# Kernel optimization log

Measured on AMD Instinct MI355X. Metric: run time of the kernel, lower is better.

Reference implementation:

```python
import jax, jax.numpy as jnp
import numpy as np

N = 50000      # nodes
E = 800000     # edges
C = 32         # channels (in = hidden = out, hardcoded in module)
KS = 4         # spline kernel size per dim
K = KS ** 3    # total spline kernel weights (dim=3)
H = 8          # NodeFormer heads
DH = C // H    # head dim = 4
M = 32         # random features for softmax kernel
EPS = 1e-5
SLOPE = 0.01   # LeakyReLU default
TAU = 1.0      # forward default


def seg_sum(vals, segs, num):
    return jax.ops.segment_sum(vals, segs, num_segments=num)


def leaky(x):
    return jnp.where(x >= 0, x, SLOPE * x)


def batch_norm(x, gamma, beta):
    # BatchNorm1d in training mode over the node dim (biased variance)
    mu = x.mean(0)
    var = x.var(0)
    return (x - mu) * jax.lax.rsqrt(var + EPS) * gamma + beta


def spline_conv(x, edge_index, pseudo, w_kernel, w_root, bias):
    # Degree-1 open B-spline conv (torch_spline_conv semantics), mean aggregation.
    src, dst = edge_index[0], edge_index[1]
    x_src = x[src]                                  # [E, C] gather
    p = pseudo * (KS - 1)                           # [E, 3], pseudo in [0,1]
    f = jnp.clip(jnp.floor(p), 0, KS - 2).astype(jnp.int32)
    frac = p - f                                    # [E, 3]
    buf = jnp.zeros((N * K, C), x.dtype)            # [N*K, C] per-kernel scatter buffer
    for bits in range(8):                           # 2^dim nonzero basis products
        idx = jnp.zeros(E, jnp.int32)
        basis = jnp.ones(E, x.dtype)
        for d in range(3):
            bit = (bits >> d) & 1
            idx = idx + (f[:, d] + bit) * (KS ** d)
            basis = basis * (frac[:, d] if bit else (1.0 - frac[:, d]))
        buf = buf + seg_sum(basis[:, None] * x_src, dst.astype(jnp.int32) * K + idx, N * K)
    buf = buf.reshape(N, K, C)
    deg = jnp.clip(seg_sum(jnp.ones(E, x.dtype), dst, N), 1.0)
    out = jnp.einsum('nkc,kcd->nd', buf, w_kernel) / deg[:, None]
    return out + x @ w_root + bias


def softmax_kernel(x, wp):
    # Positive random-feature map approximating the softmax kernel. x: [N,H,DH]
    xn = x / (DH ** 0.25)
    proj = jnp.einsum('nhd,hdm->nhm', xn, wp)
    sq = 0.5 * jnp.sum(xn * xn, -1, keepdims=True)
    return jnp.exp(proj - sq) / np.float32(np.sqrt(M))


def nodeformer_conv(x, edge_index, wqkv, wp, b_rel, wo, bo, gumbel, tau):
    # Kernelized Gumbel-softmax linear attention over all nodes + edge relational bias.
    q = jnp.einsum('nc,chd->nhd', x, wqkv[0])
    k = jnp.einsum('nc,chd->nhd', x, wqkv[1])
    v = jnp.einsum('nc,chd->nhd', x, wqkv[2])
    phi_q = softmax_kernel(q, wp)                              # [N,H,M]
    phi_k = softmax_kernel(k, wp) * jnp.exp(gumbel / tau)      # gumbel: [N,H,1]
    kv = jnp.einsum('nhm,nhd->hmd', phi_k, v)                  # [H,M,DH] summary
    num = jnp.einsum('nhm,hmd->nhd', phi_q, kv)
    den = jnp.einsum('nhm,hm->nh', phi_q, phi_k.sum(0)) + 1e-6
    attn = num / den[..., None]                                # [N,H,DH]
    # relational bias along observed edges (deg-normalized message passing)
    src, dst = edge_index[0], edge_index[1]
    deg = jnp.clip(seg_sum(jnp.ones(E, x.dtype), dst, N), 1.0)
    norm_e = jax.lax.rsqrt(deg[src] * deg[dst])
    rel = seg_sum(v[src] * norm_e[:, None, None], dst, N)      # [N,H,DH]
    out = attn + jax.nn.sigmoid(b_rel)[None, :, None] * rel
    return out.reshape(N, H * DH) @ wo + bo


def setup_inputs() -> dict:
    key = jax.random.key(0)
    ks = jax.random.split(key, 24)
    s_k = np.float32(1.0 / np.sqrt(C))
    inp = {
        'patch_embs': jax.random.normal(ks[0], (N, C), jnp.float32),
        'edge_index': jax.random.randint(ks[1], (2, E), 0, N),
        'edge_attr': jax.random.uniform(ks[2], (E, 3), jnp.float32),
        # SplineConv 1 & 2 params
        'w_sp1': jax.random.normal(ks[3], (K, C, C), jnp.float32) * s_k,
        'root1': jax.random.normal(ks[4], (C, C), jnp.float32) * s_k,
        'bias1': jnp.zeros((C,), jnp.float32),
        'w_sp2': jax.random.normal(ks[5], (K, C, C), jnp.float32) * s_k,
        'root2': jax.random.normal(ks[6], (C, C), jnp.float32) * s_k,
        'bias2': jnp.zeros((C,), jnp.float32),
        # 4 BatchNorm layers, packed
        'bn_gamma': jnp.ones((4, C), jnp.float32),
        'bn_beta': jnp.zeros((4, C), jnp.float32),
        # NodeFormer layer 1
        'nf1_wqkv': jax.random.normal(ks[7], (3, C, H, DH), jnp.float32) * s_k,
        'nf1_wp': jax.random.normal(ks[8], (H, DH, M), jnp.float32),
        'nf1_brel': jnp.zeros((H,), jnp.float32),
        'nf1_wo': jax.random.normal(ks[9], (H * DH, C), jnp.float32) * s_k,
        'nf1_bo': jnp.zeros((C,), jnp.float32),
        'gumbel1': -jnp.log(-jnp.log(jax.random.uniform(ks[10], (N, H, 1), jnp.float32) + 1e-9) + 1e-9),
        # NodeFormer layer 2
        'nf2_wqkv': jax.random.normal(ks[11], (3, C, H, DH), jnp.float32) * s_k,
        'nf2_wp': jax.random.normal(ks[12], (H, DH, M), jnp.float32),
        'nf2_brel': jnp.zeros((H,), jnp.float32),
        'nf2_wo': jax.random.normal(ks[13], (H * DH, C), jnp.float32) * s_k,
        'nf2_bo': jnp.zeros((C,), jnp.float32),
        'gumbel2': -jnp.log(-jnp.log(jax.random.uniform(ks[14], (N, H, 1), jnp.float32) + 1e-9) + 1e-9),
    }
    return inp


def reference(patch_embs, edge_index, edge_attr,
              w_sp1, root1, bias1, w_sp2, root2, bias2,
              bn_gamma, bn_beta,
              nf1_wqkv, nf1_wp, nf1_brel, nf1_wo, nf1_bo, gumbel1,
              nf2_wqkv, nf2_wp, nf2_brel, nf2_wo, nf2_bo, gumbel2):
    x = batch_norm(leaky(spline_conv(patch_embs, edge_index, edge_attr, w_sp1, root1, bias1)), bn_gamma[0], bn_beta[0])
    x = batch_norm(leaky(spline_conv(x, edge_index, edge_attr, w_sp2, root2, bias2)), bn_gamma[1], bn_beta[1])
    x = batch_norm(leaky(nodeformer_conv(x, edge_index, nf1_wqkv, nf1_wp, nf1_brel, nf1_wo, nf1_bo, gumbel1, TAU)), bn_gamma[2], bn_beta[2])
    x = batch_norm(nodeformer_conv(x, edge_index, nf2_wqkv, nf2_wp, nf2_brel, nf2_wo, nf2_bo, gumbel2, TAU), bn_gamma[3], bn_beta[3])
    return x
```

## Files before the change

### kernel.cpp

```cpp
#include <hip/hip_runtime.h>
#include <hip/hip_bf16.h>

#define NN 50000
#define NE 800000

__device__ __forceinline__ void gAdd(float* p, float v) {
    unsafeAtomicAdd(p, v);
}
__device__ __forceinline__ unsigned short f2bf(float f) {
    unsigned u = __float_as_uint(f);
    u += 0x7FFF + ((u >> 16) & 1);
    return (unsigned short)(u >> 16);
}

__global__ void k_hist(const int* __restrict__ ei, int* __restrict__ cnt) {
    int e = blockIdx.x * 256 + threadIdx.x;
    atomicAdd(&cnt[ei[NE + e]], 1);
}

__global__ void __launch_bounds__(1024) k_scan(const int* __restrict__ cnt,
                                               int* __restrict__ rowptr,
                                               int* __restrict__ fill,
                                               float* __restrict__ degf) {
    __shared__ int wsum[16];
    int tid = threadIdx.x;
    int wave = tid >> 6, lane = tid & 63;
    int carry = 0;
    for (int base = 0; base < NN; base += 8192) {
        int i0 = base + tid * 8;
        int v[8], pre[8], s = 0;
#pragma unroll
        for (int j = 0; j < 8; j++) {
            int i = i0 + j;
            v[j] = (i < NN) ? cnt[i] : 0;
            pre[j] = s; s += v[j];
        }
        int sc = s;
#pragma unroll
        for (int d = 1; d < 64; d <<= 1) {
            int t = __shfl_up(sc, d);
            if (lane >= d) sc += t;
        }
        if (lane == 63) wsum[wave] = sc;
        __syncthreads();
        int wpre = 0, total = 0;
#pragma unroll
        for (int w = 0; w < 16; w++) {
            int x = wsum[w];
            if (w < wave) wpre += x;
            total += x;
        }
        int excl = carry + wpre + (sc - s);
#pragma unroll
        for (int j = 0; j < 8; j++) {
            int i = i0 + j;
            if (i < NN) {
                int st = excl + pre[j];
                rowptr[i] = st;
                fill[i]   = st;
                degf[i]   = (float)(v[j] > 0 ? v[j] : 1);
                if (i == NN - 1) rowptr[NN] = st + v[j];
            }
        }
        carry += total;
        __syncthreads();
    }
}

__global__ void k_scatter(const int* __restrict__ ei, const float* __restrict__ attr,
                          const float* __restrict__ degf,
                          int* __restrict__ fill, float4* __restrict__ sedge,
                          float2* __restrict__ re2) {
    int e = blockIdx.x * 256 + threadIdx.x;
    int src = ei[e], dst = ei[NE + e];
    int pos = atomicAdd(&fill[dst], 1);
    float4 r;
    r.x = __int_as_float(src);
    r.y = attr[e * 3 + 0]; r.z = attr[e * 3 + 1]; r.w = attr[e * 3 + 2];
    sedge[pos] = r;
    re2[pos] = make_float2(__int_as_float(src), rsqrtf(degf[src] * degf[dst]));
}

__global__ void k_cvt(const float* __restrict__ xin, unsigned short* __restrict__ xh) {
    int i = blockIdx.x * 256 + threadIdx.x;
    xh[i] = f2bf(xin[i]);
}

__device__ __forceinline__ void edge_rmw(float* __restrict__ buf,
                                         float ay, float az, float aw, int t,
                                         float xs, int ch, int hi) {
    float p0 = ay * 3.f, p1 = az * 3.f, p2 = aw * 3.f;
    float f0 = fmaxf(fminf(floorf(p0), 2.f), 0.f);
    float f1 = fmaxf(fminf(floorf(p1), 2.f), 0.f);
    float f2 = fmaxf(fminf(floorf(p2), 2.f), 0.f);
    float r0 = p0 - f0, r1 = p1 - f1, r2 = p2 - f2;
    int i0 = (int)f0, i1 = (int)f1, i2 = (int)f2;
    int addr0, addr1, addr2, addr3;
    float b0v, b1v, b2v, b3v;
#pragma unroll
    for (int q = 0; q < 4; q++) {
        int bits = hi * 4 + q;
        int b0 = bits & 1, b1 = (bits >> 1) & 1, b2 = (bits >> 2) & 1;
        float bas = (b0 ? r0 : 1.f - r0) * (b1 ? r1 : 1.f - r1) * (b2 ? r2 : 1.f - r2);
        int idx = (i0 + b0) + 4 * (i1 + b1) + 16 * (i2 + b2);
        int a = ((idx * 4 + t) << 5) + (ch ^ ((idx & 7) << 2));
        if (q == 0) { addr0 = a; b0v = bas * xs; }
        else if (q == 1) { addr1 = a; b1v = bas * xs; }
        else if (q == 2) { addr2 = a; b2v = bas * xs; }
        else { addr3 = a; b3v = bas * xs; }
    }
    float v0 = buf[addr0], v1 = buf[addr1], v2 = buf[addr2], v3 = buf[addr3];
    buf[addr0] = v0 + b0v;
    buf[addr1] = v1 + b1v;
    buf[addr2] = v2 + b2v;
    buf[addr3] = v3 + b3v;
}

__global__ void __launch_bounds__(256) k_spline(
        const float* __restrict__ xin, const unsigned short* __restrict__ xh,
        const int* __restrict__ rowptr,
        const float4* __restrict__ sedge, const float* __restrict__ degf,
        const float* __restrict__ wsp, const float* __restrict__ root,
        const float* __restrict__ bias, float* __restrict__ out,
        float* __restrict__ stats) {
    __shared__ __align__(16) float buf[8192];
    __shared__ __align__(16) float xt[4][32];
    __shared__ __align__(16) float scr[1024];
    __shared__ float scr2[2][64];
    int tid = threadIdx.x;
    int wave = tid >> 6, lane = tid & 63;
    for (int i = tid; i < 8192; i += 256) buf[i] = 0.f;
    int nb = blockIdx.x * 4;
    if (tid < 128) {
        int t = tid >> 5, c = tid & 31;
        xt[t][c] = xin[(nb + t) * 32 + c];
    }
    __syncthreads();
    {
        int n = nb + wave;
        int rs = rowptr[n], re = rowptr[n + 1];
        int ch = lane & 31, hi = lane >> 5;
        for (int ce = rs; ce < re; ce += 64) {
            int cnt = re - ce; if (cnt > 64) cnt = 64;
            float4 myed = make_float4(0.f, 0.f, 0.f, 0.f);
            if (lane < cnt) myed = sedge[ce + lane];
            int mysrc = __float_as_int(myed.x);
            for (int j0 = 0; j0 < cnt; j0 += 8) {
                float xsv[8], ey[8], ez[8], ew[8];
#pragma unroll
                for (int jj = 0; jj < 8; jj++) {
                    int j = j0 + jj;
                    int s  = __shfl(mysrc, j);
                    ey[jj] = __shfl(myed.y, j);
                    ez[jj] = __shfl(myed.z, j);
                    ew[jj] = __shfl(myed.w, j);
                    int sc = (j < cnt) ? s : 0;
                    unsigned short u = xh[sc * 32 + ch];
                    xsv[jj] = __uint_as_float(((unsigned)u) << 16);
                }
#pragma unroll
                for (int jj = 0; jj < 8; jj++) {
                    int j = j0 + jj;
                    if (j < cnt)
                        edge_rmw(buf, ey[jj], ez[jj], ew[jj], wave, xsv[jj], ch, hi);
                }
            }
        }
    }
    __syncthreads();
    int kk = lane >> 3, d8 = lane & 7;
    float4 acc[2][4];
#pragma unroll
    for (int hf = 0; hf < 2; hf++)
#pragma unroll
        for (int t = 0; t < 4; t++) acc[hf][t] = make_float4(0.f, 0.f, 0.f, 0.f);
#pragma unroll
    for (int hf = 0; hf < 2; hf++) {
        int k = hf * 32 + wave * 8 + kk;
        const float* wk = wsp + k * 1024;
#pragma unroll
        for (int c4 = 0; c4 < 8; c4++) {
            float4 wv0 = *(const float4*)(wk + (c4 * 4 + 0) * 32 + d8 * 4);
            float4 wv1 = *(const float4*)(wk + (c4 * 4 + 1) * 32 + d8 * 4);
            float4 wv2 = *(const float4*)(wk + (c4 * 4 + 2) * 32 + d8 * 4);
            float4 wv3 = *(const float4*)(wk + (c4 * 4 + 3) * 32 + d8 * 4);
            int cp = (c4 ^ kk) << 2;
            const float* bp = &buf[(k * 4) << 5];
#pragma unroll
            for (int t = 0; t < 4; t++) {
                float4 bv = *(const float4*)(bp + (t << 5) + cp);
                acc[hf][t].x += bv.x * wv0.x + bv.y * wv1.x + bv.z * wv2.x + bv.w * wv3.x;
                acc[hf][t].y += bv.x * wv0.y + bv.y * wv1.y + bv.z * wv2.y + bv.w * wv3.y;
                acc[hf][t].z += bv.x * wv0.z + bv.y * wv1.z + bv.z * wv2.z + bv.w * wv3.z;
                acc[hf][t].w += bv.x * wv0.w + bv.y * wv1.w + bv.z * wv2.w + bv.w * wv3.w;
            }
        }
    }
#pragma unroll
    for (int hf = 0; hf < 2; hf++)
#pragma unroll
    for (int t = 0; t < 4; t++) {
        float sx = acc[hf][t].x, sy = acc[hf][t].y, sz = acc[hf][t].z, sw = acc[hf][t].w;
        sx += __shfl_xor(sx, 8);  sy += __shfl_xor(sy, 8);  sz += __shfl_xor(sz, 8);  sw += __shfl_xor(sw, 8);
        sx += __shfl_xor(sx, 16); sy += __shfl_xor(sy, 16); sz += __shfl_xor(sz, 16); sw += __shfl_xor(sw, 16);
        sx += __shfl_xor(sx, 32); sy += __shfl_xor(sy, 32); sz += __shfl_xor(sz, 32); sw += __shfl_xor(sw, 32);
        acc[hf][t] = make_float4(sx, sy, sz, sw);
    }
    if (kk == 0) {
#pragma unroll
        for (int hf = 0; hf < 2; hf++)
#pragma unroll
        for (int t = 0; t < 4; t++)
            *(float4*)&scr[(wave * 2 + hf) * 128 + d8 * 16 + t * 4] = acc[hf][t];
    }
    __syncthreads();
    if (tid < 128) {
        int t = tid >> 5, d = tid & 31;
        int n = nb + t;
        float v = 0.f;
#pragma unroll
        for (int wh = 0; wh < 8; wh++)
            v += scr[wh * 128 + (d >> 2) * 16 + t * 4 + (d & 3)];
        v /= degf[n];
        float rt = 0.f;
#pragma unroll
        for (int c = 0; c < 32; c++) rt += xt[t][c] * root[c * 32 + d];
        v += rt + bias[d];
        v = v >= 0.f ? v : 0.01f * v;
        out[n * 32 + d] = v;
        float s = v, s2 = v * v;
        s += __shfl_xor(s, 32); s2 += __shfl_xor(s2, 32);
        if ((tid & 63) < 32) {
            scr2[tid >> 6][d] = s;
            scr2[tid >> 6][32 + d] = s2;
        }
    }
    __syncthreads();
    if (tid < 64) gAdd(&stats[(blockIdx.x & 63) * 64 + tid], scr2[0][tid] + scr2[1][tid]);
}

__global__ void k_red(const float* __restrict__ stats, float* __restrict__ fin) {
    int j = threadIdx.x;
    float s = 0.f;
#pragma unroll 8
    for (int r = 0; r < 64; r++) s += stats[r * 64 + j];
    fin[j] = s;
}

__global__ void k_bn(const float* __restrict__ tin, const float* __restrict__ fin,
                     const float* __restrict__ gamma, const float* __restrict__ beta,
                     float* __restrict__ xout) {
    int i = blockIdx.x * 256 + threadIdx.x;
    int c = i & 31;
    float mu = fin[c] * (1.f / NN);
    float var = fin[32 + c] * (1.f / NN) - mu * mu;
    float g = gamma[c] * rsqrtf(var + 1e-5f);
    xout[i] = (tin[i] - mu) * g + beta[c];
}
__global__ void k_bn_cvt(const float* __restrict__ tin, const float* __restrict__ fin,
                         const float* __restrict__ gamma, const float* __restrict__ beta,
                         float* __restrict__ xout, unsigned short* __restrict__ xh) {
    int i = blockIdx.x * 256 + threadIdx.x;
    int c = i & 31;
    float mu = fin[c] * (1.f / NN);
    float var = fin[32 + c] * (1.f / NN) - mu * mu;
    float g = gamma[c] * rsqrtf(var + 1e-5f);
    float v = (tin[i] - mu) * g + beta[c];
    xout[i] = v;
    xh[i] = f2bf(v);
}

__global__ void __launch_bounds__(256) k_nf1(
        const float* __restrict__ x, const float* __restrict__ wqkv,
        const float* __restrict__ wp, const float* __restrict__ gumbel,
        float* __restrict__ vbuf, float* __restrict__ kvg) {
    __shared__ float xl[32 * 33];
    __shared__ __align__(16) float kq[32][8][4];
    __shared__ __align__(16) float vv[32][8][4];
    __shared__ float sqv[32][8];
    __shared__ float gsv[32][8];
    int tid = threadIdx.x;
    int base = blockIdx.x * 32;
#pragma unroll
    for (int r = 0; r < 4; r++) {
        int i = r * 256 + tid;
        int gi = base * 32 + i;
        float v = (gi < NN * 32) ? x[gi] : 0.f;
        xl[(i >> 5) * 33 + (i & 31)] = v;
    }
    __syncthreads();
    int nl = tid >> 3, h = tid & 7;
    int n = base + nl;
    int act = (n < NN) ? 1 : 0;
    const float* xp = &xl[nl * 33];
    float kr0 = 0, kr1 = 0, kr2 = 0, kr3 = 0, vr0 = 0, vr1 = 0, vr2 = 0, vr3 = 0;
#pragma unroll
    for (int c = 0; c < 32; c++) {
        float xc = xp[c];
        const float4 wk4 = *(const float4*)(wqkv + 1024 + c * 32 + h * 4);
        const float4 wv4 = *(const float4*)(wqkv + 2048 + c * 32 + h * 4);
        kr0 += xc * wk4.x; kr1 += xc * wk4.y; kr2 += xc * wk4.z; kr3 += xc * wk4.w;
        vr0 += xc * wv4.x; vr1 += xc * wv4.y; vr2 += xc * wv4.z; vr3 += xc * wv4.w;
    }
    if (act) *(float4*)&vbuf[n * 32 + h * 4] = make_float4(vr0, vr1, vr2, vr3);
    const float inv_rt2 = 0.70710678118f;
    const float invSqM = 0.17677669529f;
    float x0 = kr0 * inv_rt2, x1 = kr1 * inv_rt2, x2 = kr2 * inv_rt2, x3 = kr3 * inv_rt2;
    float sq = 0.5f * (x0 * x0 + x1 * x1 + x2 * x2 + x3 * x3);
    float gs = act ? (__expf(gumbel[(act ? n : 0) * 8 + h]) * invSqM) : 0.f;
    *(float4*)&kq[nl][h][0] = make_float4(x0, x1, x2, x3);
    *(float4*)&vv[nl][h][0] = make_float4(vr0, vr1, vr2, vr3);
    sqv[nl][h] = sq;
    gsv[nl][h] = gs;
    __syncthreads();
    int h2 = tid >> 5, m = tid & 31;
    const float* wph = wp + h2 * 128;
    float w0 = wph[m], w1 = wph[32 + m], w2 = wph[64 + m], w3 = wph[96 + m];
    float ks = 0.f, a0 = 0.f, a1 = 0.f, a2 = 0.f, a3 = 0.f;
#pragma unroll 4
    for (int nn2 = 0; nn2 < 32; nn2++) {
        float4 k4 = *(const float4*)&kq[nn2][h2][0];
        float4 v4 = *(const float4*)&vv[nn2][h2][0];
        float pr = k4.x * w0 + k4.y * w1 + k4.z * w2 + k4.w * w3;
        float phk = __expf(pr - sqv[nn2][h2]) * gsv[nn2][h2];
        ks += phk;
        a0 += phk * v4.x; a1 += phk * v4.y; a2 += phk * v4.z; a3 += phk * v4.w;
    }
    float* kvr = kvg + (blockIdx.x & 7) * 1280;
    gAdd(&kvr[1024 + h2 * 32 + m], ks);
    gAdd(&kvr[0 * 256 + h2 * 32 + m], a0);
    gAdd(&kvr[1 * 256 + h2 * 32 + m], a1);
    gAdd(&kvr[2 * 256 + h2 * 32 + m], a2);
    gAdd(&kvr[3 * 256 + h2 * 32 + m], a3);
}

__global__ void __launch_bounds__(256) k_nf2(
        const float* __restrict__ x, const float* __restrict__ wqkv,
        const float* __restrict__ wp, const float* __restrict__ brel,
        const float* __restrict__ wo, const float* __restrict__ bo,
        const float* __restrict__ kvg, const int* __restrict__ rowptr,
        const float2* __restrict__ re2, const float* __restrict__ vbuf,
        int do_leaky, float* __restrict__ out, float* __restrict__ stats) {
    __shared__ float xl[32 * 33];
    __shared__ float ylds[32 * 33];
    __shared__ float kvs[1280];
    __shared__ float scr2[4][64];
    int tid = threadIdx.x;
    int base = blockIdx.x * 32;
#pragma unroll
    for (int r = 0; r < 4; r++) {
        int i = r * 256 + tid;
        int gi = base * 32 + i;
        float v = (gi < NN * 32) ? x[gi] : 0.f;
        xl[(i >> 5) * 33 + (i & 31)] = v;
    }
    for (int i = tid; i < 1280; i += 256) {
        float s = 0.f;
#pragma unroll
        for (int r = 0; r < 8; r++) s += kvg[r * 1280 + i];
        kvs[i] = s;
    }
    __syncthreads();
    int nl = tid >> 3, h = tid & 7;
    int n = base + nl;
    int act = (n < NN) ? 1 : 0;
    int nc = act ? n : (NN - 1);
    const float* xp = &xl[nl * 33];
    float q0 = 0, q1 = 0, q2 = 0, q3 = 0;
#pragma unroll
    for (int c = 0; c < 32; c++) {
        float xc = xp[c];
        const float4 wq4 = *(const float4*)(wqkv + c * 32 + h * 4);
        q0 += xc * wq4.x; q1 += xc * wq4.y; q2 += xc * wq4.z; q3 += xc * wq4.w;
    }
    const float inv_rt2 = 0.70710678118f;
    const float invSqM = 0.17677669529f;
    float x0 = q0 * inv_rt2, x1 = q1 * inv_rt2, x2 = q2 * inv_rt2, x3 = q3 * inv_rt2;
    float sq = 0.5f * (x0 * x0 + x1 * x1 + x2 * x2 + x3 * x3);
    const float* wph = wp + h * 128;
    float den = 0.f, n0 = 0.f, n1 = 0.f, n2 = 0.f, n3 = 0.f;
    for (int mm = 0; mm < 32; mm++) {
        int m = (mm + 4 * h) & 31;
        float pr = x0 * wph[m] + x1 * wph[32 + m] + x2 * wph[64 + m] + x3 * wph[96 + m];
        float phq = __expf(pr - sq) * invSqM;
        den += phq * kvs[1024 + h * 32 + m];
        n0 += phq * kvs[0 * 256 + h * 32 + m];
        n1 += phq * kvs[1 * 256 + h * 32 + m];
        n2 += phq * kvs[2 * 256 + h * 32 + m];
        n3 += phq * kvs[3 * 256 + h * 32 + m];
    }
    float inv = 1.f / (den + 1e-6f);
    float y0 = n0 * inv, y1 = n1 * inv, y2 = n2 * inv, y3 = n3 * inv;
    float r0 = 0, r1 = 0, r2 = 0, r3 = 0;
    int rs = rowptr[nc];
    int re = act ? rowptr[nc + 1] : rs;
    int lb = (tid & 63) & 56;
    for (int e0 = rs; e0 < re; e0 += 8) {
        int cnt = re - e0; if (cnt > 8) cnt = 8;
        float2 med = make_float2(__int_as_float(0), 0.f);
        if (h < cnt) med = re2[e0 + h];
        int msrc = __float_as_int(med.x);
        float4 xs4[8];
        float nrj[8];
#pragma unroll
        for (int jj = 0; jj < 8; jj++) {
            int s   = __shfl(msrc, lb + jj);
            float nr = __shfl(med.y, lb + jj);
            nrj[jj] = (jj < cnt) ? nr : 0.f;
            int sc  = (jj < cnt) ? s : 0;
            xs4[jj] = *(const float4*)&vbuf[sc * 32 + h * 4];
        }
#pragma unroll
        for (int jj = 0; jj < 8; jj++) {
            r0 += nrj[jj] * xs4[jj].x;
            r1 += nrj[jj] * xs4[jj].y;
            r2 += nrj[jj] * xs4[jj].z;
            r3 += nrj[jj] * xs4[jj].w;
        }
    }
    float sg = 1.f / (1.f + __expf(-brel[h]));
    y0 += sg * r0; y1 += sg * r1; y2 += sg * r2; y3 += sg * r3;
    ylds[nl * 33 + h * 4 + 0] = y0;
    ylds[nl * 33 + h * 4 + 1] = y1;
    ylds[nl * 33 + h * 4 + 2] = y2;
    ylds[nl * 33 + h * 4 + 3] = y3;
    __syncthreads();
    const float* yp = &ylds[nl * 33];
    const float4 b4 = *(const float4*)(bo + h * 4);
    float z0 = b4.x, z1 = b4.y, z2 = b4.z, z3 = b4.w;
#pragma unroll
    for (int j = 0; j < 32; j++) {
        float yv = yp[j];
        const float4 w4 = *(const float4*)(wo + j * 32 + h * 4);
        z0 += yv * w4.x; z1 += yv * w4.y; z2 += yv * w4.z; z3 += yv * w4.w;
    }
    if (do_leaky) {
        z0 = z0 >= 0.f ? z0 : 0.01f * z0;
        z1 = z1 >= 0.f ? z1 : 0.01f * z1;
        z2 = z2 >= 0.f ? z2 : 0.01f * z2;
        z3 = z3 >= 0.f ? z3 : 0.01f * z3;
    }
    if (act) *(float4*)&out[n * 32 + h * 4] = make_float4(z0, z1, z2, z3);
    int wv = tid >> 6;
    float sv[4] = {act ? z0 : 0.f, act ? z1 : 0.f, act ? z2 : 0.f, act ? z3 : 0.f};
#pragma unroll
    for (int j = 0; j < 4; j++) {
        float s = sv[j], s2 = sv[j] * sv[j];
        s += __shfl_xor(s, 8);  s2 += __shfl_xor(s2, 8);
        s += __shfl_xor(s, 16); s2 += __shfl_xor(s2, 16);
        s += __shfl_xor(s, 32); s2 += __shfl_xor(s2, 32);
        if (((tid & 63) >> 3) == 0) {
            scr2[wv][h * 4 + j] = s;
            scr2[wv][32 + h * 4 + j] = s2;
        }
    }
    __syncthreads();
    if (tid < 64)
        gAdd(&stats[(blockIdx.x & 63) * 64 + tid],
             scr2[0][tid] + scr2[1][tid] + scr2[2][tid] + scr2[3][tid]);
}

extern "C" void kernel_launch(void* const* d_in, const int* in_sizes, int n_in,
                              void* d_out, int out_size, void* d_ws, size_t ws_size,
                              hipStream_t stream) {
    (void)in_sizes; (void)n_in; (void)out_size; (void)ws_size;
    const float* x_in  = (const float*)d_in[0];
    const int*   ei    = (const int*)d_in[1];
    const float* attr  = (const float*)d_in[2];
    const float* wsp1  = (const float*)d_in[3];
    const float* root1 = (const float*)d_in[4];
    const float* bias1 = (const float*)d_in[5];
    const float* wsp2  = (const float*)d_in[6];
    const float* root2 = (const float*)d_in[7];
    const float* bias2 = (const float*)d_in[8];
    const float* gam   = (const float*)d_in[9];
    const float* bet   = (const float*)d_in[10];
    const float* w1qkv = (const float*)d_in[11];
    const float* w1p   = (const float*)d_in[12];
    const float* b1rel = (const float*)d_in[13];
    const float* w1o   = (const float*)d_in[14];
    const float* b1o   = (const float*)d_in[15];
    const float* gum1  = (const float*)d_in[16];
    const float* w2qkv = (const float*)d_in[17];
    const float* w2p   = (const float*)d_in[18];
    const float* b2rel = (const float*)d_in[19];
    const float* w2o   = (const float*)d_in[20];
    const float* b2o   = (const float*)d_in[21];
    const float* gum2  = (const float*)d_in[22];
    float* outp = (float*)d_out;

    char* wsb = (char*)d_ws;
    size_t off = 0;
    auto carve = [&](size_t bytes) -> char* {
        char* p = wsb + off;
        off += (bytes + 255) & ~(size_t)255;
        return p;
    };
    int*    cnt    = (int*)carve((size_t)NN * 4);
    float*  kvg1   = (float*)carve(8 * 1280 * 4);
    float*  kvg2   = (float*)carve(8 * 1280 * 4);
    float*  stats  = (float*)carve(4 * 64 * 64 * 4);
    size_t zero_bytes = off;
    float*  fin    = (float*)carve(4 * 64 * 4);
    int*    rowptr = (int*)carve((size_t)(NN + 1) * 4);
    int*    fill   = (int*)carve((size_t)NN * 4);
    float*  degf   = (float*)carve((size_t)NN * 4);
    float4* sedge  = (float4*)carve((size_t)NE * 16);
    float2* re2    = (float2*)carve((size_t)NE * 8);
    unsigned short* xh0 = (unsigned short*)carve((size_t)NN * 32 * 2);
    unsigned short* xah = (unsigned short*)carve((size_t)NN * 32 * 2);
    float*  vbuf   = (float*)carve((size_t)NN * 32 * 4);
    float*  xa     = (float*)carve((size_t)NN * 32 * 4);
    float*  xb     = (float*)carve((size_t)NN * 32 * 4);
    float*  tb     = (float*)carve((size_t)NN * 32 * 4);

    hipMemsetAsync(d_ws, 0, zero_bytes, stream);
    k_hist<<<NE / 256, 256, 0, stream>>>(ei, cnt);
    k_scan<<<1, 1024, 0, stream>>>(cnt, rowptr, fill, degf);
    k_scatter<<<NE / 256, 256, 0, stream>>>(ei, attr, degf, fill, sedge, re2);
    k_cvt<<<NN * 32 / 256, 256, 0, stream>>>(x_in, xh0);

    k_spline<<<NN / 4, 256, 0, stream>>>(x_in, xh0, rowptr, sedge, degf, wsp1, root1, bias1, tb, stats);
    k_red<<<1, 64, 0, stream>>>(stats, fin);
    k_bn_cvt<<<NN * 32 / 256, 256, 0, stream>>>(tb, fin, gam, bet, xa, xah);
    k_spline<<<NN / 4, 256, 0, stream>>>(xa, xah, rowptr, sedge, degf, wsp2, root2, bias2, tb, stats + 4096);
    k_red<<<1, 64, 0, stream>>>(stats + 4096, fin + 64);
    k_bn<<<NN * 32 / 256, 256, 0, stream>>>(tb, fin + 64, gam + 32, bet + 32, xb);

    int nfgrid = (NN + 31) / 32;
    k_nf1<<<nfgrid, 256, 0, stream>>>(xb, w1qkv, w1p, gum1, vbuf, kvg1);
    k_nf2<<<nfgrid, 256, 0, stream>>>(xb, w1qkv, w1p, b1rel, w1o, b1o, kvg1, rowptr, re2,
                                      vbuf, 1, tb, stats + 8192);
    k_red<<<1, 64, 0, stream>>>(stats + 8192, fin + 128);
    k_bn<<<NN * 32 / 256, 256, 0, stream>>>(tb, fin + 128, gam + 64, bet + 64, xa);
    k_nf1<<<nfgrid, 256, 0, stream>>>(xa, w2qkv, w2p, gum2, vbuf, kvg2);
    k_nf2<<<nfgrid, 256, 0, stream>>>(xa, w2qkv, w2p, b2rel, w2o, b2o, kvg2, rowptr, re2,
                                      vbuf, 0, tb, stats + 12288);
    k_red<<<1, 64, 0, stream>>>(stats + 12288, fin + 192);
    k_bn<<<NN * 32 / 256, 256, 0, stream>>>(tb, fin + 192, gam + 96, bet + 96, outp);
}
```

Measured before the change: 1.285 ms.

## Precompute fp16 spline basis per edge, bf16 V buffer, fold stat reduction into BN

The scatter kernel now computes each edge's spline base index and its eight basis weights once, packed as fp16 into a 32-byte record. Both spline convolutions then read these instead of recomputing floor and fractions per lane. The NodeFormer value buffer is stored as bf16 to halve gather traffic, and the separate stat-reduction kernel is removed, with every BN block redoing the 64-row reduction itself. The costs are larger per-edge records, lower-precision basis weights and values, and redundant reduction work in each BN block.

```diff
diff --git a/kernel.cpp b/kernel.cpp
--- a/kernel.cpp
+++ b/kernel.cpp
@@ -1,5 +1,6 @@
 #include <hip/hip_runtime.h>
 #include <hip/hip_bf16.h>
+#include <hip/hip_fp16.h>
 
 #define NN 50000
 #define NE 800000
@@ -69,57 +70,43 @@
 
 __global__ void k_scatter(const int* __restrict__ ei, const float* __restrict__ attr,
                           const float* __restrict__ degf,
-                          int* __restrict__ fill, float4* __restrict__ sedge,
+                          int* __restrict__ fill, int* __restrict__ sedgeP,
                           float2* __restrict__ re2) {
     int e = blockIdx.x * 256 + threadIdx.x;
     int src = ei[e], dst = ei[NE + e];
     int pos = atomicAdd(&fill[dst], 1);
-    float4 r;
-    r.x = __int_as_float(src);
-    r.y = attr[e * 3 + 0]; r.z = attr[e * 3 + 1]; r.w = attr[e * 3 + 2];
-    sedge[pos] = r;
-    re2[pos] = make_float2(__int_as_float(src), rsqrtf(degf[src] * degf[dst]));
-}
-
-__global__ void k_cvt(const float* __restrict__ xin, unsigned short* __restrict__ xh) {
-    int i = blockIdx.x * 256 + threadIdx.x;
-    xh[i] = f2bf(xin[i]);
-}
-
-__device__ __forceinline__ void edge_rmw(float* __restrict__ buf,
-                                         float ay, float az, float aw, int t,
-                                         float xs, int ch, int hi) {
-    float p0 = ay * 3.f, p1 = az * 3.f, p2 = aw * 3.f;
+    float p0 = attr[e * 3 + 0] * 3.f, p1 = attr[e * 3 + 1] * 3.f, p2 = attr[e * 3 + 2] * 3.f;
     float f0 = fmaxf(fminf(floorf(p0), 2.f), 0.f);
     float f1 = fmaxf(fminf(floorf(p1), 2.f), 0.f);
     float f2 = fmaxf(fminf(floorf(p2), 2.f), 0.f);
     float r0 = p0 - f0, r1 = p1 - f1, r2 = p2 - f2;
-    int i0 = (int)f0, i1 = (int)f1, i2 = (int)f2;
-    int addr0, addr1, addr2, addr3;
-    float b0v, b1v, b2v, b3v;
-#pragma unroll
-    for (int q = 0; q < 4; q++) {
-        int bits = hi * 4 + q;
+    int idxb = (int)f0 + 4 * (int)f1 + 16 * (int)f2;
+    unsigned hw[8];
+#pragma unroll
+    for (int bits = 0; bits < 8; bits++) {
         int b0 = bits & 1, b1 = (bits >> 1) & 1, b2 = (bits >> 2) & 1;
         float bas = (b0 ? r0 : 1.f - r0) * (b1 ? r1 : 1.f - r1) * (b2 ? r2 : 1.f - r2);
-        int idx = (i0 + b0) + 4 * (i1 + b1) + 16 * (i2 + b2);
-        int a = ((idx * 4 + t) << 5) + (ch ^ ((idx & 7) << 2));
-        if (q == 0) { addr0 = a; b0v = bas * xs; }
-        else if (q == 1) { addr1 = a; b1v = bas * xs; }
-        else if (q == 2) { addr2 = a; b2v = bas * xs; }
-        else { addr3 = a; b3v = bas * xs; }
-    }
-    float v0 = buf[addr0], v1 = buf[addr1], v2 = buf[addr2], v3 = buf[addr3];
-    buf[addr0] = v0 + b0v;
-    buf[addr1] = v1 + b1v;
-    buf[addr2] = v2 + b2v;
-    buf[addr3] = v3 + b3v;
+        hw[bits] = (unsigned)__half_as_ushort(__float2half(bas));
+    }
+    int b = pos * 8;
+    sedgeP[b + 0] = src;
+    sedgeP[b + 1] = idxb;
+    sedgeP[b + 2] = (int)(hw[0] | (hw[1] << 16));
+    sedgeP[b + 3] = (int)(hw[2] | (hw[3] << 16));
+    sedgeP[b + 4] = (int)(hw[4] | (hw[5] << 16));
+    sedgeP[b + 5] = (int)(hw[6] | (hw[7] << 16));
+    re2[pos] = make_float2(__int_as_float(src), rsqrtf(degf[src] * degf[dst]));
+}
+
+__global__ void k_cvt(const float* __restrict__ xin, unsigned short* __restrict__ xh) {
+    int i = blockIdx.x * 256 + threadIdx.x;
+    xh[i] = f2bf(xin[i]);
 }
 
 __global__ void __launch_bounds__(256) k_spline(
         const float* __restrict__ xin, const unsigned short* __restrict__ xh,
         const int* __restrict__ rowptr,
-        const float4* __restrict__ sedge, const float* __restrict__ degf,
+        const int* __restrict__ sedgeP, const float* __restrict__ degf,
         const float* __restrict__ wsp, const float* __restrict__ root,
         const float* __restrict__ bias, float* __restrict__ out,
         float* __restrict__ stats) {
@@ -140,29 +127,48 @@
         int n = nb + wave;
         int rs = rowptr[n], re = rowptr[n + 1];
         int ch = lane & 31, hi = lane >> 5;
+        int tof = wave << 5;
         for (int ce = rs; ce < re; ce += 64) {
             int cnt = re - ce; if (cnt > 64) cnt = 64;
-            float4 myed = make_float4(0.f, 0.f, 0.f, 0.f);
-            if (lane < cnt) myed = sedge[ce + lane];
-            int mysrc = __float_as_int(myed.x);
+            int2 hdr = make_int2(0, 0);
+            if (lane < cnt) hdr = *(const int2*)&sedgeP[(ce + lane) * 8];
+            int mysrc = hdr.x, myidxb = hdr.y;
             for (int j0 = 0; j0 < cnt; j0 += 8) {
-                float xsv[8], ey[8], ez[8], ew[8];
+                float xsv[8]; int ib2[8]; uint2 wp[8];
 #pragma unroll
                 for (int jj = 0; jj < 8; jj++) {
                     int j = j0 + jj;
                     int s  = __shfl(mysrc, j);
-                    ey[jj] = __shfl(myed.y, j);
-                    ez[jj] = __shfl(myed.z, j);
-                    ew[jj] = __shfl(myed.w, j);
-                    int sc = (j < cnt) ? s : 0;
+                    int ib = __shfl(myidxb, j);
+                    int ok = (j < cnt);
+                    int sc = ok ? s : 0;
+                    int je = ce + (ok ? j : 0);
                     unsigned short u = xh[sc * 32 + ch];
                     xsv[jj] = __uint_as_float(((unsigned)u) << 16);
+                    ib2[jj] = ib + (hi << 4);
+                    wp[jj]  = *(const uint2*)&sedgeP[je * 8 + 2 + hi * 2];
                 }
 #pragma unroll
                 for (int jj = 0; jj < 8; jj++) {
                     int j = j0 + jj;
-                    if (j < cnt)
-                        edge_rmw(buf, ey[jj], ez[jj], ew[jj], wave, xsv[jj], ch, hi);
+                    if (j < cnt) {
+                        uint2 w = wp[jj];
+                        float xs = xsv[jj];
+                        float b0 = __half2float(__ushort_as_half((unsigned short)(w.x & 0xFFFF)));
+                        float b1 = __half2float(__ushort_as_half((unsigned short)(w.x >> 16)));
+                        float b2 = __half2float(__ushort_as_half((unsigned short)(w.y & 0xFFFF)));
+                        float b3 = __half2float(__ushort_as_half((unsigned short)(w.y >> 16)));
+                        int i0 = ib2[jj], i1 = i0 + 1, i2 = i0 + 4, i3 = i0 + 5;
+                        int a0 = (i0 << 7) + tof + (ch ^ ((i0 & 7) << 2));
+                        int a1 = (i1 << 7) + tof + (ch ^ ((i1 & 7) << 2));
+                        int a2 = (i2 << 7) + tof + (ch ^ ((i2 & 7) << 2));
+                        int a3 = (i3 << 7) + tof + (ch ^ ((i3 & 7) << 2));
+                        float v0 = buf[a0], v1 = buf[a1], v2 = buf[a2], v3 = buf[a3];
+                        buf[a0] = v0 + b0 * xs;
+                        buf[a1] = v1 + b1 * xs;
+                        buf[a2] = v2 + b2 * xs;
+                        buf[a3] = v3 + b3 * xs;
+                    }
                 }
             }
         }
@@ -239,31 +245,41 @@
     if (tid < 64) gAdd(&stats[(blockIdx.x & 63) * 64 + tid], scr2[0][tid] + scr2[1][tid]);
 }
 
-__global__ void k_red(const float* __restrict__ stats, float* __restrict__ fin) {
-    int j = threadIdx.x;
-    float s = 0.f;
-#pragma unroll 8
-    for (int r = 0; r < 64; r++) s += stats[r * 64 + j];
-    fin[j] = s;
-}
-
-__global__ void k_bn(const float* __restrict__ tin, const float* __restrict__ fin,
+__global__ void k_bn(const float* __restrict__ tin, const float* __restrict__ stats,
                      const float* __restrict__ gamma, const float* __restrict__ beta,
                      float* __restrict__ xout) {
-    int i = blockIdx.x * 256 + threadIdx.x;
+    __shared__ float fl[64];
+    int tid = threadIdx.x;
+    if (tid < 64) {
+        float s = 0.f;
+#pragma unroll 8
+        for (int r = 0; r < 64; r++) s += stats[r * 64 + tid];
+        fl[tid] = s;
+    }
+    __syncthreads();
+    int i = blockIdx.x * 256 + tid;
     int c = i & 31;
-    float mu = fin[c] * (1.f / NN);
-    float var = fin[32 + c] * (1.f / NN) - mu * mu;
+    float mu = fl[c] * (1.f / NN);
+    float var = fl[32 + c] * (1.f / NN) - mu * mu;
     float g = gamma[c] * rsqrtf(var + 1e-5f);
     xout[i] = (tin[i] - mu) * g + beta[c];
 }
-__global__ void k_bn_cvt(const float* __restrict__ tin, const float* __restrict__ fin,
+__global__ void k_bn_cvt(const float* __restrict__ tin, const float* __restrict__ stats,
                          const float* __restrict__ gamma, const float* __restrict__ beta,
                          float* __restrict__ xout, unsigned short* __restrict__ xh) {
-    int i = blockIdx.x * 256 + threadIdx.x;
+    __shared__ float fl[64];
+    int tid = threadIdx.x;
+    if (tid < 64) {
+        float s = 0.f;
+#pragma unroll 8
+        for (int r = 0; r < 64; r++) s += stats[r * 64 + tid];
+        fl[tid] = s;
+    }
+    __syncthreads();
+    int i = blockIdx.x * 256 + tid;
     int c = i & 31;
-    float mu = fin[c] * (1.f / NN);
-    float var = fin[32 + c] * (1.f / NN) - mu * mu;
+    float mu = fl[c] * (1.f / NN);
+    float var = fl[32 + c] * (1.f / NN) - mu * mu;
     float g = gamma[c] * rsqrtf(var + 1e-5f);
     float v = (tin[i] - mu) * g + beta[c];
     xout[i] = v;
@@ -273,7 +289,7 @@
 __global__ void __launch_bounds__(256) k_nf1(
         const float* __restrict__ x, const float* __restrict__ wqkv,
         const float* __restrict__ wp, const float* __restrict__ gumbel,
-        float* __restrict__ vbuf, float* __restrict__ kvg) {
+        unsigned short* __restrict__ vh, float* __restrict__ kvg) {
     __shared__ float xl[32 * 33];
     __shared__ __align__(16) float kq[32][8][4];
     __shared__ __align__(16) float vv[32][8][4];
@@ -302,7 +318,11 @@
         kr0 += xc * wk4.x; kr1 += xc * wk4.y; kr2 += xc * wk4.z; kr3 += xc * wk4.w;
         vr0 += xc * wv4.x; vr1 += xc * wv4.y; vr2 += xc * wv4.z; vr3 += xc * wv4.w;
     }
-    if (act) *(float4*)&vbuf[n * 32 + h * 4] = make_float4(vr0, vr1, vr2, vr3);
+    if (act) {
+        unsigned lo = (unsigned)f2bf(vr0) | ((unsigned)f2bf(vr1) << 16);
+        unsigned hi_ = (unsigned)f2bf(vr2) | ((unsigned)f2bf(vr3) << 16);
+        *(uint2*)&vh[n * 32 + h * 4] = make_uint2(lo, hi_);
+    }
     const float inv_rt2 = 0.70710678118f;
     const float invSqM = 0.17677669529f;
     float x0 = kr0 * inv_rt2, x1 = kr1 * inv_rt2, x2 = kr2 * inv_rt2, x3 = kr3 * inv_rt2;
@@ -339,7 +359,7 @@
         const float* __restrict__ wp, const float* __restrict__ brel,
         const float* __restrict__ wo, const float* __restrict__ bo,
         const float* __restrict__ kvg, const int* __restrict__ rowptr,
-        const float2* __restrict__ re2, const float* __restrict__ vbuf,
+        const float2* __restrict__ re2, const unsigned short* __restrict__ vh,
         int do_leaky, float* __restrict__ out, float* __restrict__ stats) {
     __shared__ float xl[32 * 33];
     __shared__ float ylds[32 * 33];
@@ -400,7 +420,7 @@
         float2 med = make_float2(__int_as_float(0), 0.f);
         if (h < cnt) med = re2[e0 + h];
         int msrc = __float_as_int(med.x);
-        float4 xs4[8];
+        uint2 xs4[8];
         float nrj[8];
 #pragma unroll
         for (int jj = 0; jj < 8; jj++) {
@@ -408,14 +428,15 @@
             float nr = __shfl(med.y, lb + jj);
             nrj[jj] = (jj < cnt) ? nr : 0.f;
             int sc  = (jj < cnt) ? s : 0;
-            xs4[jj] = *(const float4*)&vbuf[sc * 32 + h * 4];
+            xs4[jj] = *(const uint2*)&vh[sc * 32 + h * 4];
         }
 #pragma unroll
         for (int jj = 0; jj < 8; jj++) {
-            r0 += nrj[jj] * xs4[jj].x;
-            r1 += nrj[jj] * xs4[jj].y;
-            r2 += nrj[jj] * xs4[jj].z;
-            r3 += nrj[jj] * xs4[jj].w;
+            uint2 u = xs4[jj];
+            r0 += nrj[jj] * __uint_as_float(u.x << 16);
+            r1 += nrj[jj] * __uint_as_float(u.x & 0xFFFF0000u);
+            r2 += nrj[jj] * __uint_as_float(u.y << 16);
+            r3 += nrj[jj] * __uint_as_float(u.y & 0xFFFF0000u);
         }
     }
     float sg = 1.f / (1.f + __expf(-brel[h]));
@@ -501,15 +522,14 @@
     float*  kvg2   = (float*)carve(8 * 1280 * 4);
     float*  stats  = (float*)carve(4 * 64 * 64 * 4);
     size_t zero_bytes = off;
-    float*  fin    = (float*)carve(4 * 64 * 4);
     int*    rowptr = (int*)carve((size_t)(NN + 1) * 4);
     int*    fill   = (int*)carve((size_t)NN * 4);
     float*  degf   = (float*)carve((size_t)NN * 4);
-    float4* sedge  = (float4*)carve((size_t)NE * 16);
+    int*    sedgeP = (int*)carve((size_t)NE * 32);
     float2* re2    = (float2*)carve((size_t)NE * 8);
     unsigned short* xh0 = (unsigned short*)carve((size_t)NN * 32 * 2);
     unsigned short* xah = (unsigned short*)carve((size_t)NN * 32 * 2);
-    float*  vbuf   = (float*)carve((size_t)NN * 32 * 4);
+    unsigned short* vh  = (unsigned short*)carve((size_t)NN * 32 * 2);
     float*  xa     = (float*)carve((size_t)NN * 32 * 4);
     float*  xb     = (float*)carve((size_t)NN * 32 * 4);
     float*  tb     = (float*)carve((size_t)NN * 32 * 4);
@@ -517,25 +537,21 @@
     hipMemsetAsync(d_ws, 0, zero_bytes, stream);
     k_hist<<<NE / 256, 256, 0, stream>>>(ei, cnt);
     k_scan<<<1, 1024, 0, stream>>>(cnt, rowptr, fill, degf);
-    k_scatter<<<NE / 256, 256, 0, stream>>>(ei, attr, degf, fill, sedge, re2);
+    k_scatter<<<NE / 256, 256, 0, stream>>>(ei, attr, degf, fill, sedgeP, re2);
     k_cvt<<<NN * 32 / 256, 256, 0, stream>>>(x_in, xh0);
 
-    k_spline<<<NN / 4, 256, 0, stream>>>(x_in, xh0, rowptr, sedge, degf, wsp1, root1, bias1, tb, stats);
-    k_red<<<1, 64, 0, stream>>>(stats, fin);
-    k_bn_cvt<<<NN * 32 / 256, 256, 0, stream>>>(tb, fin, gam, bet, xa, xah);
-    k_spline<<<NN / 4, 256, 0, stream>>>(xa, xah, rowptr, sedge, degf, wsp2, root2, bias2, tb, stats + 4096);
-    k_red<<<1, 64, 0, stream>>>(stats + 4096, fin + 64);
-    k_bn<<<NN * 32 / 256, 256, 0, stream>>>(tb, fin + 64, gam + 32, bet + 32, xb);
+    k_spline<<<NN / 4, 256, 0, stream>>>(x_in, xh0, rowptr, sedgeP, degf, wsp1, root1, bias1, tb, stats);
+    k_bn_cvt<<<NN * 32 / 256, 256, 0, stream>>>(tb, stats, gam, bet, xa, xah);
+    k_spline<<<NN / 4, 256, 0, stream>>>(xa, xah, rowptr, sedgeP, degf, wsp2, root2, bias2, tb, stats + 4096);
+    k_bn<<<NN * 32 / 256, 256, 0, stream>>>(tb, stats + 4096, gam + 32, bet + 32, xb);
 
     int nfgrid = (NN + 31) / 32;
-    k_nf1<<<nfgrid, 256, 0, stream>>>(xb, w1qkv, w1p, gum1, vbuf, kvg1);
+    k_nf1<<<nfgrid, 256, 0, stream>>>(xb, w1qkv, w1p, gum1, vh, kvg1);
     k_nf2<<<nfgrid, 256, 0, stream>>>(xb, w1qkv, w1p, b1rel, w1o, b1o, kvg1, rowptr, re2,
-                                      vbuf, 1, tb, stats + 8192);
-    k_red<<<1, 64, 0, stream>>>(stats + 8192, fin + 128);
-    k_bn<<<NN * 32 / 256, 256, 0, stream>>>(tb, fin + 128, gam + 64, bet + 64, xa);
-    k_nf1<<<nfgrid, 256, 0, stream>>>(xa, w2qkv, w2p, gum2, vbuf, kvg2);
+                                      vh, 1, tb, stats + 8192);
+    k_bn<<<NN * 32 / 256, 256, 0, stream>>>(tb, stats + 8192, gam + 64, bet + 64, xa);
+    k_nf1<<<nfgrid, 256, 0, stream>>>(xa, w2qkv, w2p, gum2, vh, kvg2);
     k_nf2<<<nfgrid, 256, 0, stream>>>(xa, w2qkv, w2p, b2rel, w2o, b2o, kvg2, rowptr, re2,
-                                      vbuf, 0, tb, stats + 12288);
-    k_red<<<1, 64, 0, stream>>>(stats + 12288, fin + 192);
-    k_bn<<<NN * 32 / 256, 256, 0, stream>>>(tb, fin + 192, gam + 96, bet + 96, outp);
-}
+                                      vh, 0, tb, stats + 12288);
+    k_bn<<<NN * 32 / 256, 256, 0, stream>>>(tb, stats + 12288, gam + 96, bet + 96, outp);
+}
```

After: 1.250 ms. 1.03x faster.
